# Performance work log

Hardware: AMD Instinct MI355X
Metric: run time of the kernel (lower is better)

Reference implementation:

```python
import jax, jax.numpy as jnp
import numpy as np

B, C, H, W = 2, 256, 100, 100
G, P = 4, 8
CG = C // G  # 64 per-group channels
EPS = 1e-5


def setup_inputs() -> dict:
    key = jax.random.key(0)
    ks = jax.random.split(key, 5)
    bev_query = jax.random.normal(ks[0], (B, C, H, W), dtype=jnp.float32)
    pts = jax.random.normal(ks[1], (B, H * W, 1, P, C), dtype=jnp.float32)
    conv_w = jax.random.normal(ks[2], (G * CG * CG, C), dtype=jnp.float32) * (1.0 / np.sqrt(C))
    conv_b = jax.random.normal(ks[3], (G * CG * CG,), dtype=jnp.float32) * 0.02
    ln_g = jnp.ones((CG,), dtype=jnp.float32)
    ln_b = jnp.zeros((CG,), dtype=jnp.float32)
    proj_w = jax.random.normal(ks[4], (CG, CG * P), dtype=jnp.float32) * (1.0 / np.sqrt(CG * P))
    proj_b = jnp.zeros((CG,), dtype=jnp.float32)
    return {"bev_query": bev_query, "pts": pts, "conv_w": conv_w, "conv_b": conv_b,
            "ln_g": ln_g, "ln_b": ln_b, "proj_w": proj_w, "proj_b": proj_b}


def reference(bev_query, pts, conv_w, conv_b, ln_g, ln_b, proj_w, proj_b):
    b, c, h, w = bev_query.shape
    q = h * w
    # pts: b q 1 p c -> b q p c
    pts = jnp.squeeze(pts, axis=2)
    # 1x1 conv parameter generator: b c h w -> b (g c1 c2) h w
    param = jnp.einsum('bchw,oc->bohw', bev_query, conv_w) + conv_b[None, :, None, None]
    # 'b (g c1 c2) h w -> (b g) (h w) c1 c2'
    param = param.reshape(b, G, CG, CG, q).transpose(0, 1, 4, 2, 3).reshape(b * G, q, CG, CG)
    # 'b q p (g c) -> (b g) q p c'
    pts_g = pts.reshape(b, q, P, G, CG).transpose(0, 3, 1, 2, 4).reshape(b * G, q, P, CG)
    # batched per-pixel matmul: (bg,q,p,c1) @ (bg,q,c1,c2) -> (bg,q,p,c2)
    mixed = jnp.matmul(pts_g, param)
    # LayerNorm over last dim + ReLU
    mu = jnp.mean(mixed, axis=-1, keepdims=True)
    var = jnp.var(mixed, axis=-1, keepdims=True)
    normed = (mixed - mu) * jax.lax.rsqrt(var + EPS) * ln_g + ln_b
    act = jax.nn.relu(normed)
    # 'b q p c -> b q (p c)' then linear
    flat = act.reshape(b * G, q, P * CG)
    out = jnp.einsum('bqi,oi->bqo', flat, proj_w) + proj_b
    # '(b g) (h w) c -> b (g c) h w'
    out = out.reshape(b, G, q, CG).transpose(0, 1, 3, 2).reshape(b, G * CG, h, w)
    return out
```

## Files before the change

kernel.cpp:

```cpp
#include <hip/hip_runtime.h>
#include <hip/hip_bf16.h>
#include <stdint.h>

#define QTOT 10000
#define MPAD 10240
#define CDIM 256
#define ODIM 16384
#define RTOT 20096

using f32x4  = __attribute__((ext_vector_type(4))) float;
using bf16x8 = __attribute__((ext_vector_type(8))) short;

#define GLOAD_LDS(gp, lp) __builtin_amdgcn_global_load_lds(                     \
    (const __attribute__((address_space(1))) unsigned int*)(gp),                \
    (__attribute__((address_space(3))) unsigned int*)(lp), 16, 0, 0)

static __device__ __forceinline__ short f2bs(float x) {
  __hip_bfloat16 h = __float2bfloat16(x);
  return *(short*)&h;
}

__global__ void cvt_f32_bf16(const float* __restrict__ s, __hip_bfloat16* __restrict__ d, int n) {
  for (int i = blockIdx.x * blockDim.x + threadIdx.x; i < n; i += gridDim.x * blockDim.x)
    d[i] = __float2bfloat16(s[i]);
}

__global__ void cvt_permute_cw(const float* __restrict__ s, __hip_bfloat16* __restrict__ d, int n) {
  for (int i = blockIdx.x * blockDim.x + threadIdx.x; i < n; i += gridDim.x * blockDim.x) {
    int rn = i >> 8, c = i & 255;
    int ro = (rn & ~4095) | ((rn & 63) << 6) | ((rn >> 6) & 63);
    d[i] = __float2bfloat16(s[ro * 256 + c]);
  }
}

__global__ __launch_bounds__(256) void transpose_bev(const float* __restrict__ bev,
                                                     __hip_bfloat16* __restrict__ bevT) {
  __shared__ float tl[32][33];
  int tx = threadIdx.x, ty = threadIdx.y;
  int q0 = blockIdx.x * 32, c0 = blockIdx.y * 32, b = blockIdx.z;
#pragma unroll
  for (int i = 0; i < 4; ++i) {
    int c = c0 + ty + i * 8, q = q0 + tx;
    tl[ty + i * 8][tx] = (q < QTOT) ? bev[((size_t)b * CDIM + c) * QTOT + q] : 0.0f;
  }
  __syncthreads();
#pragma unroll
  for (int i = 0; i < 4; ++i) {
    int q = q0 + ty + i * 8, c = c0 + tx;
    bevT[((size_t)b * MPAD + q) * CDIM + c] = __float2bfloat16(tl[tx][ty + i * 8]);
  }
}

__global__ __launch_bounds__(256) void gemm_param(const __hip_bfloat16* __restrict__ A,
                                                  const __hip_bfloat16* __restrict__ Bw,
                                                  const float* __restrict__ convb,
                                                  __hip_bfloat16* __restrict__ P) {
  __shared__ __align__(16) unsigned char lsA[2][16384];
  __shared__ __align__(16) unsigned char lsB[2][16384];
  int t = threadIdx.x, lane = t & 63, w = t >> 6;
  int bm = blockIdx.x, bn = blockIdx.y;
  int wm = (w >> 1) * 64, wn = (w & 1) * 64;
  int srow = lane >> 3;
  int kbs  = ((lane & 7) ^ srow) * 8;
  const __hip_bfloat16* pA = A  + (size_t)(bm * 128 + w * 32 + srow) * CDIM + kbs;
  const __hip_bfloat16* pB = Bw + (size_t)(bn * 128 + w * 32 + srow) * CDIM + kbs;
  f32x4 acc[4][4] = {};

#define STAGE_P(buf, kt) do {                                                   \
    _Pragma("unroll")                                                           \
    for (int i = 0; i < 4; ++i) {                                               \
      GLOAD_LDS(pA + (size_t)i * 8 * CDIM + (kt), lsA[buf] + (w * 4 + i) * 1024); \
      GLOAD_LDS(pB + (size_t)i * 8 * CDIM + (kt), lsB[buf] + (w * 4 + i) * 1024); \
    } } while (0)

  STAGE_P(0, 0);
  asm volatile("s_waitcnt vmcnt(0)" ::: "memory");
  __builtin_amdgcn_s_barrier();
#pragma unroll
  for (int kt = 0; kt < 4; ++kt) {
    const int cur = kt & 1;
    if (kt < 3) STAGE_P(cur ^ 1, (kt + 1) * 64);
    __builtin_amdgcn_sched_barrier(0);
#pragma unroll
    for (int kk = 0; kk < 2; ++kk) {
      int kb = kk * 64 + ((lane >> 4) << 4);
      bf16x8 af[4], bfr[4];
#pragma unroll
      for (int mi = 0; mi < 4; ++mi) {
        int row = wm + mi * 16 + (lane & 15);
        af[mi] = *(const bf16x8*)(lsA[cur] + ((row * 128 + kb) ^ ((row & 7) << 4)));
      }
#pragma unroll
      for (int ni = 0; ni < 4; ++ni) {
        int row = wn + ni * 16 + (lane & 15);
        bfr[ni] = *(const bf16x8*)(lsB[cur] + ((row * 128 + kb) ^ ((row & 7) << 4)));
      }
#pragma unroll
      for (int mi = 0; mi < 4; ++mi)
#pragma unroll
        for (int ni = 0; ni < 4; ++ni)
          acc[mi][ni] = __builtin_amdgcn_mfma_f32_16x16x32_bf16(af[mi], bfr[ni], acc[mi][ni], 0, 0, 0);
    }
    __builtin_amdgcn_sched_barrier(0);
    if (kt < 3) asm volatile("s_waitcnt vmcnt(0)" ::: "memory");
    __builtin_amdgcn_s_barrier();
    __builtin_amdgcn_sched_barrier(0);
  }
#pragma unroll
  for (int ni = 0; ni < 4; ++ni) {
    int col = bn * 128 + wn + ni * 16 + (lane & 15);
    int o_old = (col & ~4095) | ((col & 63) << 6) | ((col >> 6) & 63);
    float cb = convb[o_old];
#pragma unroll
    for (int mi = 0; mi < 4; ++mi) {
      int rb = bm * 128 + wm + mi * 16 + ((lane >> 4) << 2);
#pragma unroll
      for (int r = 0; r < 4; ++r)
        P[(size_t)(rb + r) * ODIM + col] = __float2bfloat16(acc[mi][ni][r] + cb);
    }
  }
#undef STAGE_P
}

__global__ __launch_bounds__(256) void mix_mfma(const __hip_bfloat16* __restrict__ P,
                                                const float* __restrict__ pts,
                                                const float* __restrict__ lng,
                                                const float* __restrict__ lnb,
                                                __hip_bfloat16* __restrict__ act,
                                                int b, int q0) {
  __shared__ __align__(16) float ptsl[8 * 264];
  int t = threadIdx.x, lane = t & 63, g = t >> 6;
  int row = blockIdx.x;
  size_t rq = (size_t)b * QTOT + q0 + row;
  {
    const float4* ps = (const float4*)(pts + rq * 2048);
#pragma unroll
    for (int i = 0; i < 2; ++i) {
      int v = i * 256 + t;
      float4 val = ps[v];
      int p = v >> 6, c = (v & 63) * 4;
      *(float4*)(ptsl + p * 264 + c) = val;
    }
  }
  __syncthreads();
  int l15 = lane & 15, hi = lane >> 4;
  bf16x8 bfr[2];
#pragma unroll
  for (int kk = 0; kk < 2; ++kk) {
    bf16x8 v = {};
    if (l15 < 8) {
      const float* src = ptsl + l15 * 264 + g * 64 + kk * 32 + hi * 8;
#pragma unroll
      for (int j = 0; j < 8; ++j) v[j] = f2bs(src[j]);
    }
    bfr[kk] = v;
  }
  const __hip_bfloat16* Ap = P + (size_t)row * ODIM + g * 4096;
  f32x4 acc[4] = {};
#pragma unroll
  for (int kk = 0; kk < 2; ++kk)
#pragma unroll
    for (int mi = 0; mi < 4; ++mi) {
      bf16x8 a = *(const bf16x8*)(Ap + (size_t)(mi * 16 + l15) * 64 + kk * 32 + hi * 8);
      acc[mi] = __builtin_amdgcn_mfma_f32_16x16x32_bf16(a, bfr[kk], acc[mi], 0, 0, 0);
    }
  float s = 0.f, ss = 0.f;
#pragma unroll
  for (int mi = 0; mi < 4; ++mi)
#pragma unroll
    for (int r = 0; r < 4; ++r) { float v = acc[mi][r]; s += v; ss = fmaf(v, v, ss); }
  s += __shfl_xor(s, 16);  ss += __shfl_xor(ss, 16);
  s += __shfl_xor(s, 32);  ss += __shfl_xor(ss, 32);
  float mu  = s * 0.015625f;
  float var = ss * 0.015625f - mu * mu;
  float rs  = rsqrtf(var + 1e-5f);
  if (l15 < 8) {
    short* ab = (short*)act + ((size_t)g * RTOT + rq) * 512 + l15 * 64;
#pragma unroll
    for (int mi = 0; mi < 4; ++mi) {
      int c2 = mi * 16 + hi * 4;
      float4 gg = *(const float4*)(lng + c2);
      float4 bb = *(const float4*)(lnb + c2);
      short4 o;
      o.x = f2bs(fmaxf(0.f, (acc[mi][0] - mu) * rs * gg.x + bb.x));
      o.y = f2bs(fmaxf(0.f, (acc[mi][1] - mu) * rs * gg.y + bb.y));
      o.z = f2bs(fmaxf(0.f, (acc[mi][2] - mu) * rs * gg.z + bb.z));
      o.w = f2bs(fmaxf(0.f, (acc[mi][3] - mu) * rs * gg.w + bb.w));
      *(short4*)(ab + c2) = o;
    }
  }
}

__global__ __launch_bounds__(256) void gemm_proj(const __hip_bfloat16* __restrict__ act,
                                                 const __hip_bfloat16* __restrict__ Bp,
                                                 const float* __restrict__ projb,
                                                 float* __restrict__ outT) {
  __shared__ __align__(16) unsigned char lsA[2][16384];
  __shared__ __align__(16) unsigned char lsB[2][8192];
  int t = threadIdx.x, lane = t & 63, w = t >> 6;
  int bm = blockIdx.x, g = blockIdx.y;
  int wm = (w >> 1) * 64, wn = (w & 1) * 32;
  int srow = lane >> 3;
  int kbs  = ((lane & 7) ^ srow) * 8;
  const __hip_bfloat16* A  = act + (size_t)g * RTOT * 512;
  const __hip_bfloat16* pA = A  + (size_t)(bm * 128 + w * 32 + srow) * 512 + kbs;
  const __hip_bfloat16* pB = Bp + (size_t)(w * 16 + srow) * 512 + kbs;
  f32x4 acc[4][2] = {};

#define STAGE_Q(buf, kt) do {                                                   \
    _Pragma("unroll")                                                           \
    for (int i = 0; i < 4; ++i)                                                 \
      GLOAD_LDS(pA + (size_t)i * 8 * 512 + (kt), lsA[buf] + (w * 4 + i) * 1024); \
    _Pragma("unroll")                                                           \
    for (int j = 0; j < 2; ++j)                                                 \
      GLOAD_LDS(pB + (size_t)j * 8 * 512 + (kt), lsB[buf] + (w * 2 + j) * 1024); \
    } while (0)

  STAGE_Q(0, 0);
  asm volatile("s_waitcnt vmcnt(0)" ::: "memory");
  __builtin_amdgcn_s_barrier();
#pragma unroll
  for (int kt = 0; kt < 8; ++kt) {
    const int cur = kt & 1;
    if (kt < 7) STAGE_Q(cur ^ 1, (kt + 1) * 64);
    __builtin_amdgcn_sched_barrier(0);
#pragma unroll
    for (int kk = 0; kk < 2; ++kk) {
      int kb = kk * 64 + ((lane >> 4) << 4);
      bf16x8 af[4], bfr[2];
#pragma unroll
      for (int mi = 0; mi < 4; ++mi) {
        int row = wm + mi * 16 + (lane & 15);
        af[mi] = *(const bf16x8*)(lsA[cur] + ((row * 128 + kb) ^ ((row & 7) << 4)));
      }
#pragma unroll
      for (int ni = 0; ni < 2; ++ni) {
        int row = wn + ni * 16 + (lane & 15);
        bfr[ni] = *(const bf16x8*)(lsB[cur] + ((row * 128 + kb) ^ ((row & 7) << 4)));
      }
#pragma unroll
      for (int mi = 0; mi < 4; ++mi)
#pragma unroll
        for (int ni = 0; ni < 2; ++ni)
          acc[mi][ni] = __builtin_amdgcn_mfma_f32_16x16x32_bf16(af[mi], bfr[ni], acc[mi][ni], 0, 0, 0);
    }
    __builtin_amdgcn_sched_barrier(0);
    if (kt < 7) asm volatile("s_waitcnt vmcnt(0)" ::: "memory");
    __builtin_amdgcn_s_barrier();
    __builtin_amdgcn_sched_barrier(0);
  }
#pragma unroll
  for (int ni = 0; ni < 2; ++ni) {
    int o = wn + ni * 16 + (lane & 15);
    float pb = projb[o];
#pragma unroll
    for (int mi = 0; mi < 4; ++mi) {
      int rb = bm * 128 + wm + mi * 16 + ((lane >> 4) << 2);
#pragma unroll
      for (int r = 0; r < 4; ++r) {
        int rg = rb + r;
        if (rg < 2 * QTOT)
          outT[(size_t)rg * CDIM + g * 64 + o] = acc[mi][ni][r] + pb;
      }
    }
  }
#undef STAGE_Q
}

__global__ __launch_bounds__(256) void transpose_out(const float* __restrict__ outT,
                                                     float* __restrict__ out) {
  __shared__ float tl[32][33];
  int tx = threadIdx.x, ty = threadIdx.y;
  int q0 = blockIdx.x * 32, c0 = blockIdx.y * 32, b = blockIdx.z;
#pragma unroll
  for (int i = 0; i < 4; ++i) {
    int q = q0 + ty + i * 8, c = c0 + tx;
    tl[ty + i * 8][tx] = (q < QTOT) ? outT[((size_t)b * QTOT + q) * CDIM + c] : 0.0f;
  }
  __syncthreads();
#pragma unroll
  for (int i = 0; i < 4; ++i) {
    int c = c0 + ty + i * 8, q = q0 + tx;
    if (q < QTOT) out[((size_t)b * CDIM + c) * QTOT + q] = tl[tx][ty + i * 8];
  }
}

extern "C" void kernel_launch(void* const* d_in, const int* in_sizes, int n_in,
                              void* d_out, int out_size, void* d_ws, size_t ws_size,
                              hipStream_t stream) {
  const float* bev = (const float*)d_in[0];
  const float* pts = (const float*)d_in[1];
  const float* cw  = (const float*)d_in[2];
  const float* cb  = (const float*)d_in[3];
  const float* lng = (const float*)d_in[4];
  const float* lnb = (const float*)d_in[5];
  const float* pw  = (const float*)d_in[6];
  const float* pb  = (const float*)d_in[7];
  float* out = (float*)d_out;

  char* ws = (char*)d_ws;
  size_t off = 0;
  auto carve = [&](size_t bytes) -> char* {
    char* p = ws + off;
    off += (bytes + 255) & ~(size_t)255;
    return p;
  };
  __hip_bfloat16* cw_bf = (__hip_bfloat16*)carve((size_t)ODIM * CDIM * 2);
  __hip_bfloat16* bevT  = (__hip_bfloat16*)carve((size_t)2 * MPAD * CDIM * 2);
  __hip_bfloat16* pw_bf = (__hip_bfloat16*)carve((size_t)64 * 512 * 2);
  float* outT           = (float*)carve((size_t)2 * QTOT * CDIM * 4);
  __hip_bfloat16* act   = (__hip_bfloat16*)carve((size_t)4 * RTOT * 512 * 2);
  size_t fixed = off;

  int CH = 128;
  const int ladder[4] = {2560, 1280, 640, 128};
  for (int i = 0; i < 4; ++i) {
    size_t need = fixed + (((size_t)ladder[i] * ODIM * 2 + 255) & ~(size_t)255);
    if (need <= ws_size) { CH = ladder[i]; break; }
  }
  __hip_bfloat16* param = (__hip_bfloat16*)carve((size_t)CH * ODIM * 2);

  cvt_permute_cw<<<4096, 256, 0, stream>>>(cw, cw_bf, ODIM * CDIM);
  cvt_f32_bf16<<<128, 256, 0, stream>>>(pw, pw_bf, 64 * 512);
  transpose_bev<<<dim3(MPAD / 32, CDIM / 32, 2), dim3(32, 8), 0, stream>>>(bev, bevT);

  int nchunks = (QTOT + CH - 1) / CH;
  for (int b = 0; b < 2; ++b) {
    for (int c = 0; c < nchunks; ++c) {
      int q0 = c * CH;
      int nvalid = QTOT - q0;
      if (nvalid > CH) nvalid = CH;
      const __hip_bfloat16* Ab = bevT + ((size_t)b * MPAD + q0) * CDIM;
      gemm_param<<<dim3(CH / 128, ODIM / 128), 256, 0, stream>>>(Ab, cw_bf, cb, param);
      mix_mfma<<<dim3(nvalid), 256, 0, stream>>>(param, pts, lng, lnb, act, b, q0);
    }
  }
  gemm_proj<<<dim3(RTOT / 128, 4), 256, 0, stream>>>(act, pw_bf, pb, outT);
  transpose_out<<<dim3((QTOT + 31) / 32, CDIM / 32, 2), dim3(32, 8), 0, stream>>>(outT, out);
}
```

Measured before the change: 537.2 us.

## Fuse output transpose into proj GEMM, swizzle param GEMM blocks, enlarge chunks

The projection GEMM now writes straight into the final b,c,h,w layout with float4 stores along q, which removes the separate transpose_out kernel and the intermediate outT buffer. The parameter GEMM remaps block IDs across 8 groups (an XCD-style swizzle) so blocks that share data are placed together. The chunk-size ladder now tries 5120 first, which halves the number of gemm_param/mix launches when the workspace allows it. The risks are that the swizzle may not suit the cache topology and that a larger param buffer reduces L2 reuse between the two kernels.

```diff
diff --git a/kernel.cpp b/kernel.cpp
--- a/kernel.cpp
+++ b/kernel.cpp
@@ -54,11 +54,15 @@
 __global__ __launch_bounds__(256) void gemm_param(const __hip_bfloat16* __restrict__ A,
                                                   const __hip_bfloat16* __restrict__ Bw,
                                                   const float* __restrict__ convb,
-                                                  __hip_bfloat16* __restrict__ P) {
+                                                  __hip_bfloat16* __restrict__ P,
+                                                  int nbm) {
   __shared__ __align__(16) unsigned char lsA[2][16384];
   __shared__ __align__(16) unsigned char lsB[2][16384];
   int t = threadIdx.x, lane = t & 63, w = t >> 6;
-  int bm = blockIdx.x, bn = blockIdx.y;
+  int id = blockIdx.x + nbm * blockIdx.y;
+  int total = nbm * gridDim.y;
+  int nid = (total & 7) ? id : ((id & 7) * (total >> 3) + (id >> 3));
+  int bm = nid % nbm, bn = nid / nbm;
   int wm = (w >> 1) * 64, wn = (w & 1) * 64;
   int srow = lane >> 3;
   int kbs  = ((lane & 7) ^ srow) * 8;
@@ -194,7 +198,7 @@
 __global__ __launch_bounds__(256) void gemm_proj(const __hip_bfloat16* __restrict__ act,
                                                  const __hip_bfloat16* __restrict__ Bp,
                                                  const float* __restrict__ projb,
-                                                 float* __restrict__ outT) {
+                                                 float* __restrict__ out) {
   __shared__ __align__(16) unsigned char lsA[2][16384];
   __shared__ __align__(16) unsigned char lsB[2][8192];
   int t = threadIdx.x, lane = t & 63, w = t >> 6;
@@ -252,37 +256,29 @@
 #pragma unroll
   for (int ni = 0; ni < 2; ++ni) {
     int o = wn + ni * 16 + (lane & 15);
-    float pb = projb[o];
+    int c = g * 64 + o;
+    float pbv = projb[o];
 #pragma unroll
     for (int mi = 0; mi < 4; ++mi) {
-      int rb = bm * 128 + wm + mi * 16 + ((lane >> 4) << 2);
-#pragma unroll
-      for (int r = 0; r < 4; ++r) {
-        int rg = rb + r;
-        if (rg < 2 * QTOT)
-          outT[(size_t)rg * CDIM + g * 64 + o] = acc[mi][ni][r] + pb;
+      int rg = bm * 128 + wm + mi * 16 + ((lane >> 4) << 2);
+      float4 o4;
+      o4.x = acc[mi][ni][0] + pbv; o4.y = acc[mi][ni][1] + pbv;
+      o4.z = acc[mi][ni][2] + pbv; o4.w = acc[mi][ni][3] + pbv;
+      if (rg + 3 < QTOT) {
+        *(float4*)(out + (size_t)c * QTOT + rg) = o4;
+      } else if (rg >= QTOT && rg + 3 < 2 * QTOT) {
+        *(float4*)(out + (size_t)(CDIM + c) * QTOT + (rg - QTOT)) = o4;
+      } else {
+#pragma unroll
+        for (int r = 0; r < 4; ++r) {
+          int q = rg + r;
+          if (q < QTOT)          out[(size_t)c * QTOT + q] = (&o4.x)[r];
+          else if (q < 2 * QTOT) out[(size_t)(CDIM + c) * QTOT + (q - QTOT)] = (&o4.x)[r];
+        }
       }
     }
   }
 #undef STAGE_Q
-}
-
-__global__ __launch_bounds__(256) void transpose_out(const float* __restrict__ outT,
-                                                     float* __restrict__ out) {
-  __shared__ float tl[32][33];
-  int tx = threadIdx.x, ty = threadIdx.y;
-  int q0 = blockIdx.x * 32, c0 = blockIdx.y * 32, b = blockIdx.z;
-#pragma unroll
-  for (int i = 0; i < 4; ++i) {
-    int q = q0 + ty + i * 8, c = c0 + tx;
-    tl[ty + i * 8][tx] = (q < QTOT) ? outT[((size_t)b * QTOT + q) * CDIM + c] : 0.0f;
-  }
-  __syncthreads();
-#pragma unroll
-  for (int i = 0; i < 4; ++i) {
-    int c = c0 + ty + i * 8, q = q0 + tx;
-    if (q < QTOT) out[((size_t)b * CDIM + c) * QTOT + q] = tl[tx][ty + i * 8];
-  }
 }
 
 extern "C" void kernel_launch(void* const* d_in, const int* in_sizes, int n_in,
@@ -308,12 +304,11 @@
   __hip_bfloat16* cw_bf = (__hip_bfloat16*)carve((size_t)ODIM * CDIM * 2);
   __hip_bfloat16* bevT  = (__hip_bfloat16*)carve((size_t)2 * MPAD * CDIM * 2);
   __hip_bfloat16* pw_bf = (__hip_bfloat16*)carve((size_t)64 * 512 * 2);
-  float* outT           = (float*)carve((size_t)2 * QTOT * CDIM * 4);
   __hip_bfloat16* act   = (__hip_bfloat16*)carve((size_t)4 * RTOT * 512 * 2);
   size_t fixed = off;
 
   int CH = 128;
-  const int ladder[4] = {2560, 1280, 640, 128};
+  const int ladder[4] = {5120, 2560, 1280, 128};
   for (int i = 0; i < 4; ++i) {
     size_t need = fixed + (((size_t)ladder[i] * ODIM * 2 + 255) & ~(size_t)255);
     if (need <= ws_size) { CH = ladder[i]; break; }
@@ -324,6 +319,7 @@
   cvt_f32_bf16<<<128, 256, 0, stream>>>(pw, pw_bf, 64 * 512);
   transpose_bev<<<dim3(MPAD / 32, CDIM / 32, 2), dim3(32, 8), 0, stream>>>(bev, bevT);
 
+  int nbm = CH / 128;
   int nchunks = (QTOT + CH - 1) / CH;
   for (int b = 0; b < 2; ++b) {
     for (int c = 0; c < nchunks; ++c) {
@@ -331,10 +327,9 @@
       int nvalid = QTOT - q0;
       if (nvalid > CH) nvalid = CH;
       const __hip_bfloat16* Ab = bevT + ((size_t)b * MPAD + q0) * CDIM;
-      gemm_param<<<dim3(CH / 128, ODIM / 128), 256, 0, stream>>>(Ab, cw_bf, cb, param);
+      gemm_param<<<dim3(nbm, ODIM / 128), 256, 0, stream>>>(Ab, cw_bf, cb, param, nbm);
       mix_mfma<<<dim3(nvalid), 256, 0, stream>>>(param, pts, lng, lnb, act, b, q0);
     }
   }
-  gemm_proj<<<dim3(RTOT / 128, 4), 256, 0, stream>>>(act, pw_bf, pb, outT);
-  transpose_out<<<dim3((QTOT + 31) / 32, CDIM / 32, 2), dim3(32, 8), 0, stream>>>(outT, out);
-}
+  gemm_proj<<<dim3(RTOT / 128, 4), 256, 0, stream>>>(act, pw_bf, pb, out);
+}
```

Measured after the change: 719.2 us. +33.9%, slower.
